# Kernel optimization log

Hardware: AMD Instinct MI355X
Metric: run time of the kernel (lower is better)

## Reference

```python
import jax, jax.numpy as jnp
import numpy as np

D = 1024
H = 16
DFF = 4096
EPS = 1e-5


def layernorm(x, g, b):
    m = jnp.mean(x, axis=-1, keepdims=True)
    v = jnp.var(x, axis=-1, keepdims=True)
    return (x - m) * jax.lax.rsqrt(v + EPS) * g + b


def setup_inputs() -> dict:
    key = jax.random.key(0)
    ks = jax.random.split(key, 6)
    B, T = 2, 2048
    s = 0.02
    return {
        "x": jax.random.normal(ks[0], (B, T, D), dtype=jnp.float32),
        "W_qkv": jax.random.normal(ks[1], (D, 3 * D), dtype=jnp.float32) * s,
        "W_proj": jax.random.normal(ks[2], (D, D), dtype=jnp.float32) * s,
        "W_fc1": jax.random.normal(ks[3], (D, DFF), dtype=jnp.float32) * s,
        "W_fc2": jax.random.normal(ks[4], (DFF, D), dtype=jnp.float32) * s,
        "ln1_g": jnp.ones((D,), jnp.float32),
        "ln1_b": jnp.zeros((D,), jnp.float32),
        "ln2_g": jnp.ones((D,), jnp.float32),
        "ln2_b": jnp.zeros((D,), jnp.float32),
    }


def reference(x, W_qkv, W_proj, W_fc1, W_fc2, ln1_g, ln1_b, ln2_g, ln2_b):
    B, T, C = x.shape
    hd = C // H

    # --- attention sublayer (pre-norm) ---
    h = layernorm(x, ln1_g, ln1_b)
    qkv = h @ W_qkv                                  # [B,T,3C]
    q, k, v = jnp.split(qkv, 3, axis=-1)
    q = q.reshape(B, T, H, hd).transpose(0, 2, 1, 3)  # [B,H,T,hd]
    k = k.reshape(B, T, H, hd).transpose(0, 2, 1, 3)
    v = v.reshape(B, T, H, hd).transpose(0, 2, 1, 3)
    att = jnp.einsum('bhqd,bhkd->bhqk', q, k) * (1.0 / np.sqrt(hd))
    causal = jnp.tril(jnp.ones((T, T), dtype=bool))
    att = jnp.where(causal, att, jnp.float32(-jnp.inf))
    att = jax.nn.softmax(att, axis=-1)
    y = jnp.einsum('bhqk,bhkd->bhqd', att, v)        # [B,H,T,hd]
    y = y.transpose(0, 2, 1, 3).reshape(B, T, C)
    x = x + y @ W_proj

    # --- MLP sublayer (pre-norm) ---
    h = layernorm(x, ln2_g, ln2_b)
    h = jax.nn.gelu(h @ W_fc1, approximate=False)
    x = x + h @ W_fc2
    return x
```

## Files before the change

### kernel.cpp

```cpp
#include <hip/hip_runtime.h>
#include <hip/hip_bf16.h>
#include <math.h>

typedef __bf16 bf16;
typedef __bf16 bf16x4 __attribute__((ext_vector_type(4)));
typedef __bf16 bf16x8 __attribute__((ext_vector_type(8)));
typedef float f32x4 __attribute__((ext_vector_type(4)));
typedef unsigned int u32;

#define MFMA_BF16(a, b, c) __builtin_amdgcn_mfma_f32_16x16x32_bf16(a, b, c, 0, 0, 0)
#define ASYNC16(g, l)                                                                   \
    __builtin_amdgcn_global_load_lds((const __attribute__((address_space(1))) u32*)(g), \
                                     (__attribute__((address_space(3))) u32*)(l), 16, 0, 0)

__global__ __launch_bounds__(256)
void prep_kernel(const float* __restrict__ Wqkv, const float* __restrict__ Wproj,
                 const float* __restrict__ Wfc1, const float* __restrict__ Wfc2,
                 bf16* __restrict__ Wqkvt, bf16* __restrict__ Wprojt,
                 bf16* __restrict__ Wfc1t, bf16* __restrict__ Wfc2t,
                 const float* __restrict__ x, const float* __restrict__ g,
                 const float* __restrict__ bb, bf16* __restrict__ hb) {
    const int blk = blockIdx.x;
    const int tid = threadIdx.x;
    if (blk < 12288) {
        __shared__ float tile[32][33];
        const float* in; bf16* out; int rows, cols, bx, by;
        if (blk < 3072)      { in = Wqkv;  out = Wqkvt;  rows = 1024; cols = 3072; const int r = blk;        bx = r % 96;  by = r / 96; }
        else if (blk < 4096) { in = Wproj; out = Wprojt; rows = 1024; cols = 1024; const int r = blk - 3072; bx = r % 32;  by = r / 32; }
        else if (blk < 8192) { in = Wfc1;  out = Wfc1t;  rows = 1024; cols = 4096; const int r = blk - 4096; bx = r % 128; by = r / 128; }
        else                 { in = Wfc2;  out = Wfc2t;  rows = 4096; cols = 1024; const int r = blk - 8192; bx = r % 32;  by = r / 32; }
        const int tx = tid & 31, ty = tid >> 5;
        const int c0 = bx * 32, r0 = by * 32;
        #pragma unroll
        for (int j = 0; j < 4; j++)
            tile[ty + j * 8][tx] = in[(size_t)(r0 + ty + j * 8) * cols + c0 + tx];
        __syncthreads();
        #pragma unroll
        for (int j = 0; j < 4; j++)
            out[(size_t)(c0 + ty + j * 8) * rows + r0 + tx] = (bf16)tile[tx][ty + j * 8];
    } else {
        const int row = blk - 12288;
        const float4 v = reinterpret_cast<const float4*>(x)[(size_t)row * 256 + tid];
        float s = v.x + v.y + v.z + v.w;
        float sq = v.x * v.x + v.y * v.y + v.z * v.z + v.w * v.w;
        #pragma unroll
        for (int o = 32; o > 0; o >>= 1) { s += __shfl_xor(s, o); sq += __shfl_xor(sq, o); }
        __shared__ float ssum[4], ssq[4];
        const int wave = tid >> 6, lane = tid & 63;
        if (lane == 0) { ssum[wave] = s; ssq[wave] = sq; }
        __syncthreads();
        s = ssum[0] + ssum[1] + ssum[2] + ssum[3];
        sq = ssq[0] + ssq[1] + ssq[2] + ssq[3];
        const float mean = s * (1.0f / 1024.0f);
        const float var = sq * (1.0f / 1024.0f) - mean * mean;
        const float rstd = rsqrtf(var + 1e-5f);
        const float4 gv = reinterpret_cast<const float4*>(g)[tid];
        const float4 bv = reinterpret_cast<const float4*>(bb)[tid];
        bf16x4 o;
        o[0] = (bf16)((v.x - mean) * rstd * gv.x + bv.x);
        o[1] = (bf16)((v.y - mean) * rstd * gv.y + bv.y);
        o[2] = (bf16)((v.z - mean) * rstd * gv.z + bv.z);
        o[3] = (bf16)((v.w - mean) * rstd * gv.w + bv.w);
        reinterpret_cast<bf16x4*>(hb)[(size_t)row * 256 + tid] = o;
    }
}

__global__ __launch_bounds__(256)
void transpose_v(const bf16* __restrict__ qkv, bf16* __restrict__ vt) {
    __shared__ bf16 tile[32][33];
    const int tx = threadIdx.x, ty = threadIdx.y;
    const int t0 = blockIdx.x * 32;
    const int d0 = blockIdx.y * 32;
    const int bh = blockIdx.z;
    const int b = bh >> 4, h = bh & 15;
    const bf16* src = qkv + (size_t)b * 2048 * 3072 + 2048 + h * 64;
    #pragma unroll
    for (int j = 0; j < 4; j++)
        tile[ty + j * 8][tx] = src[(size_t)(t0 + ty + j * 8) * 3072 + d0 + tx];
    __syncthreads();
    #pragma unroll
    for (int j = 0; j < 4; j++)
        vt[((size_t)bh * 64 + d0 + ty + j * 8) * 2048 + t0 + tx] = tile[tx][ty + j * 8];
}

__global__ __launch_bounds__(256)
void ln_kernel(const float* __restrict__ x, const float* __restrict__ g,
               const float* __restrict__ bb, bf16* __restrict__ out) {
    const int row = blockIdx.x, tid = threadIdx.x;
    const float4 v = reinterpret_cast<const float4*>(x)[(size_t)row * 256 + tid];
    float s = v.x + v.y + v.z + v.w;
    float sq = v.x * v.x + v.y * v.y + v.z * v.z + v.w * v.w;
    #pragma unroll
    for (int o = 32; o > 0; o >>= 1) { s += __shfl_xor(s, o); sq += __shfl_xor(sq, o); }
    __shared__ float ssum[4], ssq[4];
    const int wave = tid >> 6, lane = tid & 63;
    if (lane == 0) { ssum[wave] = s; ssq[wave] = sq; }
    __syncthreads();
    s = ssum[0] + ssum[1] + ssum[2] + ssum[3];
    sq = ssq[0] + ssq[1] + ssq[2] + ssq[3];
    const float mean = s * (1.0f / 1024.0f);
    const float var = sq * (1.0f / 1024.0f) - mean * mean;
    const float rstd = rsqrtf(var + 1e-5f);
    const float4 gv = reinterpret_cast<const float4*>(g)[tid];
    const float4 bv = reinterpret_cast<const float4*>(bb)[tid];
    bf16x4 o;
    o[0] = (bf16)((v.x - mean) * rstd * gv.x + bv.x);
    o[1] = (bf16)((v.y - mean) * rstd * gv.y + bv.y);
    o[2] = (bf16)((v.z - mean) * rstd * gv.z + bv.z);
    o[3] = (bf16)((v.w - mean) * rstd * gv.w + bv.w);
    reinterpret_cast<bf16x4*>(out)[(size_t)row * 256 + tid] = o;
}

__device__ __forceinline__ float gelu_fast(float v) {
    const float vv = v * v;
    const float u = v * (1.595769122f + 0.0713548162726f * vv);
    const float t = exp2f(u * -1.4426950408889634f);
    return v / (1.0f + t);
}

template <int EPI>
__global__ __launch_bounds__(512, 1)
void gemm256(const bf16* __restrict__ A, const bf16* __restrict__ Bt,
             bf16* __restrict__ outb, int M, int N, int K) {
    __shared__ bf16 As[2][2][2][128][32];
    __shared__ bf16 Bs[2][2][2][128][32];
    const int tid = threadIdx.x;
    const int wave = tid >> 6, lane = tid & 63;
    const int lm = lane & 15, lq = lane >> 4;
    const int wr = wave >> 2, wc = wave & 3;
    const int bm = blockIdx.y * 256, bn = blockIdx.x * 256;
    const int srow = lane >> 2;
    const int sg = (((lane & 3) ^ ((lane >> 3) & 3)) * 8);
    const int pco = (lq ^ ((lm >> 1) & 3)) * 8;

    f32x4 acc[8][4];
    #pragma unroll
    for (int i = 0; i < 8; i++)
        #pragma unroll
        for (int j = 0; j < 4; j++) acc[i][j] = (f32x4){0.f, 0.f, 0.f, 0.f};

    auto stageA = [&](int db, int kt) {
        #pragma unroll
        for (int L = 0; L < 2; L++) {
            const int g = wave * 2 + L, slab = g >> 3, rg = g & 7;
            #pragma unroll
            for (int h = 0; h < 2; h++)
                ASYNC16(A + (size_t)(bm + h * 128 + rg * 16 + srow) * K + kt + slab * 32 + sg,
                        &As[db][h][slab][rg * 16][0]);
        }
    };
    auto stageB = [&](int db, int kt) {
        #pragma unroll
        for (int L = 0; L < 2; L++) {
            const int g = wave * 2 + L, slab = g >> 3, rg = g & 7;
            #pragma unroll
            for (int h = 0; h < 2; h++)
                ASYNC16(Bt + (size_t)(bn + h * 128 + rg * 16 + srow) * K + kt + slab * 32 + sg,
                        &Bs[db][h][slab][rg * 16][0]);
        }
    };
    auto loadA = [&](int db, int mq, bf16x8 (&dst)[4][2]) {
        #pragma unroll
        for (int i = 0; i < 4; i++)
            #pragma unroll
            for (int kk = 0; kk < 2; kk++)
                dst[i][kk] = *reinterpret_cast<const bf16x8*>(
                    &As[db][wr][kk][(mq * 4 + i) * 16 + lm][pco]);
    };
    auto loadB = [&](int db, int bq, bf16x8 (&dst)[2][2]) {
        #pragma unroll
        for (int j = 0; j < 2; j++)
            #pragma unroll
            for (int kk = 0; kk < 2; kk++)
                dst[j][kk] = *reinterpret_cast<const bf16x8*>(
                    &Bs[db][wc >> 1][kk][(wc & 1) * 64 + (bq * 2 + j) * 16 + lm][pco]);
    };
    auto quad = [&](int mq, int bq, bf16x8 (&a)[4][2], bf16x8 (&b)[2][2]) {
        #pragma unroll
        for (int kk = 0; kk < 2; kk++)
            #pragma unroll
            for (int i = 0; i < 4; i++)
                #pragma unroll
                for (int j = 0; j < 2; j++)
                    acc[mq * 4 + i][bq * 2 + j] =
                        MFMA_BF16(a[i][kk], b[j][kk], acc[mq * 4 + i][bq * 2 + j]);
    };

#define PHASE_SYNC()                                         \
    __builtin_amdgcn_s_barrier();                            \
    asm volatile("s_waitcnt lgkmcnt(0)" ::: "memory");       \
    __builtin_amdgcn_sched_barrier(0)

    const int NT = K >> 6;
    stageB(0, 0);  stageA(0, 0);
    stageB(1, 64); stageA(1, 64);
    asm volatile("s_waitcnt vmcnt(8)" ::: "memory");
    __builtin_amdgcn_s_barrier();
    __builtin_amdgcn_sched_barrier(0);

    bf16x8 af[4][2], b0[2][2], b1[2][2];
    for (int t = 0; t < NT; ++t) {
        const int db = t & 1;
        const int kt2 = (t + 2) * 64;
        loadA(db, 0, af);
        loadB(db, 0, b0);
        PHASE_SYNC();
        __builtin_amdgcn_s_setprio(1);
        quad(0, 0, af, b0);
        __builtin_amdgcn_s_setprio(0);
        __builtin_amdgcn_s_barrier();
        loadB(db, 1, b1);
        PHASE_SYNC();
        __builtin_amdgcn_s_setprio(1);
        quad(0, 1, af, b1);
        __builtin_amdgcn_s_setprio(0);
        __builtin_amdgcn_s_barrier();
        loadA(db, 1, af);
        if (t + 2 < NT) stageB(db, kt2);
        PHASE_SYNC();
        __builtin_amdgcn_s_setprio(1);
        quad(1, 0, af, b0);
        __builtin_amdgcn_s_setprio(0);
        __builtin_amdgcn_s_barrier();
        if (t + 2 < NT) {
            stageA(db, kt2);
            asm volatile("s_waitcnt vmcnt(8)" ::: "memory");
        } else if (t + 1 < NT) {
            asm volatile("s_waitcnt vmcnt(0)" ::: "memory");
        }
        __builtin_amdgcn_s_barrier();
        __builtin_amdgcn_sched_barrier(0);
        __builtin_amdgcn_s_setprio(1);
        quad(1, 1, af, b1);
        __builtin_amdgcn_s_setprio(0);
        __builtin_amdgcn_s_barrier();
    }
#undef PHASE_SYNC

    const int r0 = bm + wr * 128, c0 = bn + wc * 64;
    #pragma unroll
    for (int mi = 0; mi < 8; mi++)
        #pragma unroll
        for (int ni = 0; ni < 4; ni++)
            #pragma unroll
            for (int e = 0; e < 4; e++) {
                const int row = r0 + mi * 16 + lq * 4 + e;
                const int col = c0 + ni * 16 + lm;
                const float v = acc[mi][ni][e];
                const size_t idx = (size_t)row * N + col;
                if (EPI == 0) outb[idx] = (bf16)v;
                else          outb[idx] = (bf16)gelu_fast(v);
            }
}

__global__ __launch_bounds__(512, 2)
void gemm128p(const bf16* __restrict__ A, const bf16* __restrict__ Bt,
              const float* __restrict__ resid, float* __restrict__ outf,
              int M, int N, int K) {
    __shared__ bf16 As[3][128][64];
    __shared__ bf16 Bs[3][128][64];
    const int tid = threadIdx.x;
    const int wave = tid >> 6, lane = tid & 63;
    const int lm = lane & 15, lq = lane >> 4;
    const int wm = (wave >> 2) * 64, wn = (wave & 3) * 32;
    const int nwg = gridDim.x * gridDim.y;
    const int orig = blockIdx.x + gridDim.x * blockIdx.y;
    const int cpx = nwg >> 3;
    const int swz = (orig & 7) * cpx + (orig >> 3);
    const int bx = swz % gridDim.x, by = swz / gridDim.x;
    const int bm = by * 128, bn = bx * 128;
    const int lr8 = lane >> 3;
    const int lg  = ((lane & 7) ^ lr8) * 8;
    const int sa  = lm & 7;
    int co[2];
    co[0] = (lq ^ sa) * 8;
    co[1] = ((lq ^ 4) ^ sa) * 8;
    f32x4 acc[4][2];
    #pragma unroll
    for (int i = 0; i < 4; i++)
        #pragma unroll
        for (int j = 0; j < 2; j++) acc[i][j] = (f32x4){0.f, 0.f, 0.f, 0.f};

    auto stageA = [&](int s, int kt) {
        #pragma unroll
        for (int c = 0; c < 2; c++)
            ASYNC16(A + (size_t)(bm + (wave * 2 + c) * 8 + lr8) * K + kt + lg,
                    &As[s][(wave * 2 + c) * 8][0]);
    };
    auto stageB = [&](int s, int kt) {
        #pragma unroll
        for (int c = 0; c < 2; c++)
            ASYNC16(Bt + (size_t)(bn + (wave * 2 + c) * 8 + lr8) * K + kt + lg,
                    &Bs[s][(wave * 2 + c) * 8][0]);
    };

    const int NT = K >> 6;
    stageA(0, 0);  stageB(0, 0);
    stageA(1, 64); stageB(1, 64);
    asm volatile("s_waitcnt vmcnt(4)" ::: "memory");
    __builtin_amdgcn_s_barrier();
    __builtin_amdgcn_sched_barrier(0);

    int s = 0;
    for (int t = 0; t < NT; ++t) {
        const int s2 = (s + 2 >= 3) ? s - 1 : s + 2;
        const int kt2 = (t + 2) * 64;
        bf16x8 a0[4], b0[2];
        #pragma unroll
        for (int mi = 0; mi < 4; mi++)
            a0[mi] = *reinterpret_cast<const bf16x8*>(&As[s][wm + mi * 16 + lm][co[0]]);
        #pragma unroll
        for (int nj = 0; nj < 2; nj++)
            b0[nj] = *reinterpret_cast<const bf16x8*>(&Bs[s][wn + nj * 16 + lm][co[0]]);
        if (t + 2 < NT) stageA(s2, kt2);
        __builtin_amdgcn_s_barrier();
        asm volatile("s_waitcnt lgkmcnt(0)" ::: "memory");
        __builtin_amdgcn_sched_barrier(0);
        __builtin_amdgcn_s_setprio(1);
        #pragma unroll
        for (int mi = 0; mi < 4; mi++)
            #pragma unroll
            for (int nj = 0; nj < 2; nj++)
                acc[mi][nj] = MFMA_BF16(a0[mi], b0[nj], acc[mi][nj]);
        __builtin_amdgcn_s_setprio(0);
        __builtin_amdgcn_s_barrier();
        #pragma unroll
        for (int mi = 0; mi < 4; mi++)
            a0[mi] = *reinterpret_cast<const bf16x8*>(&As[s][wm + mi * 16 + lm][co[1]]);
        #pragma unroll
        for (int nj = 0; nj < 2; nj++)
            b0[nj] = *reinterpret_cast<const bf16x8*>(&Bs[s][wn + nj * 16 + lm][co[1]]);
        if (t + 2 < NT) {
            stageB(s2, kt2);
            asm volatile("s_waitcnt vmcnt(4)" ::: "memory");
        } else if (t + 1 < NT) {
            asm volatile("s_waitcnt vmcnt(0)" ::: "memory");
        }
        __builtin_amdgcn_s_barrier();
        asm volatile("s_waitcnt lgkmcnt(0)" ::: "memory");
        __builtin_amdgcn_sched_barrier(0);
        __builtin_amdgcn_s_setprio(1);
        #pragma unroll
        for (int mi = 0; mi < 4; mi++)
            #pragma unroll
            for (int nj = 0; nj < 2; nj++)
                acc[mi][nj] = MFMA_BF16(a0[mi], b0[nj], acc[mi][nj]);
        __builtin_amdgcn_s_setprio(0);
        __builtin_amdgcn_s_barrier();
        s = (s == 2) ? 0 : s + 1;
    }

    const int r0 = bm + wm, c0 = bn + wn;
    #pragma unroll
    for (int i = 0; i < 4; i++)
        #pragma unroll
        for (int j = 0; j < 2; j++)
            #pragma unroll
            for (int e = 0; e < 4; e++) {
                const int row = r0 + i * 16 + lq * 4 + e;
                const int col = c0 + j * 16 + lm;
                const size_t idx = (size_t)row * N + col;
                outf[idx] = resid[idx] + acc[i][j][e];
            }
}

__global__ __launch_bounds__(256)
void attn_kernel(const bf16* __restrict__ qkv, const bf16* __restrict__ vt,
                 bf16* __restrict__ y) {
    __shared__ bf16 Ks[64][68];
    __shared__ bf16 Vt[64][68];
    __shared__ bf16 Ps[4][16][68];
    const int tid = threadIdx.x, wave = tid >> 6, lane = tid & 63;
    const int lm = lane & 15, lq = lane >> 4;
    const int h = blockIdx.y, b = blockIdx.z;
    const size_t base = (size_t)b * 2048 * 3072;
    const bf16* Kbase = qkv + base + 1024 + h * 64;
    const bf16* Vbase = vt + ((size_t)(b * 16 + h) * 64) * 2048;
    const int skey = tid >> 3, sch = (tid & 7) * 8;
    const float k1 = 0.18033688011112042f;

    bf16x8 ones;
    #pragma unroll
    for (int j = 0; j < 8; j++) ones[j] = (lm == 0) ? (bf16)1.0f : (bf16)0.0f;

    for (int ph = 0; ph < 2; ph++) {
        const int qt = ph ? (int)blockIdx.x : 31 - (int)blockIdx.x;

        const int qrow = qt * 64 + wave * 16 + lm;
        const bf16* qp = qkv + base + (size_t)qrow * 3072 + h * 64 + lq * 8;
        bf16x8 aq0 = *reinterpret_cast<const bf16x8*>(qp);
        bf16x8 aq1 = *reinterpret_cast<const bf16x8*>(qp + 32);
        #pragma unroll
        for (int j = 0; j < 8; j++) {
            aq0[j] = (bf16)((float)aq0[j] * k1);
            aq1[j] = (bf16)((float)aq1[j] * k1);
        }

        f32x4 Oc[4], Ol;
        #pragma unroll
        for (int nt = 0; nt < 4; nt++) Oc[nt] = (f32x4){0.f, 0.f, 0.f, 0.f};
        Ol = (f32x4){0.f, 0.f, 0.f, 0.f};

        bf16x8 pk0, pk1, pv0, pv1;
        {
            const bf16* kp = Kbase + (size_t)skey * 3072 + sch;
            pk0 = *reinterpret_cast<const bf16x8*>(kp);
            pk1 = *reinterpret_cast<const bf16x8*>(kp + (size_t)32 * 3072);
            const bf16* vp = Vbase + (size_t)skey * 2048 + sch;
            pv0 = *reinterpret_cast<const bf16x8*>(vp);
            pv1 = *reinterpret_cast<const bf16x8*>(vp + (size_t)32 * 2048);
        }

        for (int kt2 = 0; kt2 <= qt; kt2++) {
            __syncthreads();
            *reinterpret_cast<bf16x8*>(&Ks[skey][sch])      = pk0;
            *reinterpret_cast<bf16x8*>(&Ks[skey + 32][sch]) = pk1;
            *reinterpret_cast<bf16x8*>(&Vt[skey][sch])      = pv0;
            *reinterpret_cast<bf16x8*>(&Vt[skey + 32][sch]) = pv1;
            __syncthreads();
            if (kt2 < qt) {
                const bf16* kp = Kbase + (size_t)((kt2 + 1) * 64 + skey) * 3072 + sch;
                pk0 = *reinterpret_cast<const bf16x8*>(kp);
                pk1 = *reinterpret_cast<const bf16x8*>(kp + (size_t)32 * 3072);
                const bf16* vp = Vbase + (size_t)skey * 2048 + (kt2 + 1) * 64 + sch;
                pv0 = *reinterpret_cast<const bf16x8*>(vp);
                pv1 = *reinterpret_cast<const bf16x8*>(vp + (size_t)32 * 2048);
            }

            f32x4 Sc[4];
            #pragma unroll
            for (int nt = 0; nt < 4; nt++) Sc[nt] = (f32x4){0.f, 0.f, 0.f, 0.f};
            #pragma unroll
            for (int nt = 0; nt < 4; nt++) {
                const bf16x8 bk0 = *reinterpret_cast<const bf16x8*>(&Ks[nt * 16 + lm][lq * 8]);
                const bf16x8 bk1 = *reinterpret_cast<const bf16x8*>(&Ks[nt * 16 + lm][32 + lq * 8]);
                Sc[nt] = MFMA_BF16(aq0, bk0, Sc[nt]);
                Sc[nt] = MFMA_BF16(aq1, bk1, Sc[nt]);
            }

            const int qb = wave * 16 + lq * 4;
            #pragma unroll
            for (int e = 0; e < 4; e++) {
                #pragma unroll
                for (int nt = 0; nt < 4; nt++) {
                    float sv = Sc[nt][e];
                    if (kt2 == qt && (nt * 16 + lm) > (qb + e)) sv = -1e30f;
                    Ps[wave][lq * 4 + e][nt * 16 + lm] = (bf16)exp2f(sv);
                }
            }

            const bf16x8 ap0 = *reinterpret_cast<const bf16x8*>(&Ps[wave][lm][lq * 8]);
            const bf16x8 ap1 = *reinterpret_cast<const bf16x8*>(&Ps[wave][lm][32 + lq * 8]);
            Ol = MFMA_BF16(ap0, ones, Ol);
            Ol = MFMA_BF16(ap1, ones, Ol);
            #pragma unroll
            for (int nt = 0; nt < 4; nt++) {
                const bf16x8 bv0 = *reinterpret_cast<const bf16x8*>(&Vt[nt * 16 + lm][lq * 8]);
                const bf16x8 bv1 = *reinterpret_cast<const bf16x8*>(&Vt[nt * 16 + lm][32 + lq * 8]);
                Oc[nt] = MFMA_BF16(ap0, bv0, Oc[nt]);
                Oc[nt] = MFMA_BF16(ap1, bv1, Oc[nt]);
            }
        }

        const int qrow0 = qt * 64 + wave * 16 + lq * 4;
        float inv[4];
        #pragma unroll
        for (int e = 0; e < 4; e++) inv[e] = 1.0f / __shfl(Ol[e], lane & 48);
        #pragma unroll
        for (int nt = 0; nt < 4; nt++)
            #pragma unroll
            for (int e = 0; e < 4; e++) {
                const int row = qrow0 + e;
                y[((size_t)b * 2048 + row) * 1024 + h * 64 + nt * 16 + lm] = (bf16)(Oc[nt][e] * inv[e]);
            }
    }
}

extern "C" void kernel_launch(void* const* d_in, const int* in_sizes, int n_in,
                              void* d_out, int out_size, void* d_ws, size_t ws_size,
                              hipStream_t stream) {
    const float* x     = (const float*)d_in[0];
    const float* Wqkv  = (const float*)d_in[1];
    const float* Wproj = (const float*)d_in[2];
    const float* Wfc1  = (const float*)d_in[3];
    const float* Wfc2  = (const float*)d_in[4];
    const float* ln1g  = (const float*)d_in[5];
    const float* ln1b  = (const float*)d_in[6];
    const float* ln2g  = (const float*)d_in[7];
    const float* ln2b  = (const float*)d_in[8];
    float* out = (float*)d_out;
    char* ws = (char*)d_ws;

    bf16*  Wqkvt  = (bf16*)(ws);
    bf16*  Wprojt = (bf16*)(ws + 6291456);
    bf16*  Wfc1t  = (bf16*)(ws + 8388608);
    bf16*  Wfc2t  = (bf16*)(ws + 16777216);
    bf16*  hb     = (bf16*)(ws + 25165824);
    bf16*  vt     = (bf16*)(ws + 25165824);
    bf16*  qkv    = (bf16*)(ws + 33554432);
    bf16*  yb     = (bf16*)(ws + 58720256);
    float* x1     = (float*)(ws + 67108864);
    bf16*  h3     = (bf16*)(ws + 33554432);

    const dim3 tb(32, 8);
    prep_kernel<<<dim3(16384), dim3(256), 0, stream>>>(Wqkv, Wproj, Wfc1, Wfc2,
                                                       Wqkvt, Wprojt, Wfc1t, Wfc2t,
                                                       x, ln1g, ln1b, hb);
    gemm256<0><<<dim3(12, 16), dim3(512), 0, stream>>>(hb, Wqkvt, qkv, 4096, 3072, 1024);
    transpose_v<<<dim3(64, 2, 32), tb, 0, stream>>>(qkv, vt);
    attn_kernel<<<dim3(16, 16, 2), dim3(256), 0, stream>>>(qkv, vt, yb);
    gemm128p<<<dim3(8, 32), dim3(512), 0, stream>>>(yb, Wprojt, x, x1, 4096, 1024, 1024);
    ln_kernel<<<dim3(4096), dim3(256), 0, stream>>>(x1, ln2g, ln2b, hb);
    gemm256<2><<<dim3(16, 16), dim3(512), 0, stream>>>(hb, Wfc1t, h3, 4096, 4096, 1024);
    gemm128p<<<dim3(8, 32), dim3(512), 0, stream>>>(h3, Wfc2t, x1, out, 4096, 1024, 4096);
}
```

Measured before the change: 325.8 us.

## Split-K the FC2 GEMM with atomic accumulation into residual-initialized output

Replaces the final FC2 GEMM (K=4096, 256 workgroups) with a split-K version that uses two K halves, doubling the grid to 512 workgroups to fill more CUs. The output is first initialized with the residual through a device-to-device memcpy, and each split atomically adds its partial tile. This trades an extra 16MB copy and float atomics (with nondeterministic summation order) for better occupancy and shorter per-block K loops.

```diff
diff --git a/kernel.cpp b/kernel.cpp
--- a/kernel.cpp
+++ b/kernel.cpp
@@ -364,6 +364,106 @@
             }
 }
 
+__global__ __launch_bounds__(512, 2)
+void gemm128sk(const bf16* __restrict__ A, const bf16* __restrict__ Bt,
+               float* __restrict__ outf, int M, int N, int K, int klen) {
+    __shared__ bf16 As[2][128][64];
+    __shared__ bf16 Bs[2][128][64];
+    const int tid = threadIdx.x;
+    const int wave = tid >> 6, lane = tid & 63;
+    const int lm = lane & 15, lq = lane >> 4;
+    const int wm = (wave >> 2) * 64, wn = (wave & 3) * 32;
+    const int nwg = gridDim.x * gridDim.y;
+    const int orig = blockIdx.x + gridDim.x * blockIdx.y;
+    const int cpx = nwg >> 3;
+    const int swz = (orig & 7) * cpx + (orig >> 3);
+    const int bx = swz % gridDim.x, by = swz / gridDim.x;
+    const int bm = by * 128, bn = bx * 128;
+    const int kbase = blockIdx.z * klen;
+    const int lr8 = lane >> 3;
+    const int lg  = ((lane & 7) ^ lr8) * 8;
+    const int sa  = lm & 7;
+    int co[2];
+    co[0] = (lq ^ sa) * 8;
+    co[1] = ((lq ^ 4) ^ sa) * 8;
+    f32x4 acc[4][2];
+    #pragma unroll
+    for (int i = 0; i < 4; i++)
+        #pragma unroll
+        for (int j = 0; j < 2; j++) acc[i][j] = (f32x4){0.f, 0.f, 0.f, 0.f};
+
+    auto stageA = [&](int s, int kt) {
+        #pragma unroll
+        for (int c = 0; c < 2; c++)
+            ASYNC16(A + (size_t)(bm + (wave * 2 + c) * 8 + lr8) * K + kbase + kt + lg,
+                    &As[s][(wave * 2 + c) * 8][0]);
+    };
+    auto stageB = [&](int s, int kt) {
+        #pragma unroll
+        for (int c = 0; c < 2; c++)
+            ASYNC16(Bt + (size_t)(bn + (wave * 2 + c) * 8 + lr8) * K + kbase + kt + lg,
+                    &Bs[s][(wave * 2 + c) * 8][0]);
+    };
+
+    const int NT = klen >> 6;
+    stageA(0, 0);  stageB(0, 0);
+    asm volatile("s_waitcnt vmcnt(0)" ::: "memory");
+    __builtin_amdgcn_s_barrier();
+    __builtin_amdgcn_sched_barrier(0);
+
+    for (int t = 0; t < NT; ++t) {
+        const int s = t & 1;
+        const int kt1 = (t + 1) * 64;
+        if (t + 1 < NT) { stageA(s ^ 1, kt1); stageB(s ^ 1, kt1); }
+        bf16x8 a0[4], b0[2];
+        #pragma unroll
+        for (int mi = 0; mi < 4; mi++)
+            a0[mi] = *reinterpret_cast<const bf16x8*>(&As[s][wm + mi * 16 + lm][co[0]]);
+        #pragma unroll
+        for (int nj = 0; nj < 2; nj++)
+            b0[nj] = *reinterpret_cast<const bf16x8*>(&Bs[s][wn + nj * 16 + lm][co[0]]);
+        asm volatile("s_waitcnt lgkmcnt(0)" ::: "memory");
+        __builtin_amdgcn_sched_barrier(0);
+        __builtin_amdgcn_s_setprio(1);
+        #pragma unroll
+        for (int mi = 0; mi < 4; mi++)
+            #pragma unroll
+            for (int nj = 0; nj < 2; nj++)
+                acc[mi][nj] = MFMA_BF16(a0[mi], b0[nj], acc[mi][nj]);
+        __builtin_amdgcn_s_setprio(0);
+        #pragma unroll
+        for (int mi = 0; mi < 4; mi++)
+            a0[mi] = *reinterpret_cast<const bf16x8*>(&As[s][wm + mi * 16 + lm][co[1]]);
+        #pragma unroll
+        for (int nj = 0; nj < 2; nj++)
+            b0[nj] = *reinterpret_cast<const bf16x8*>(&Bs[s][wn + nj * 16 + lm][co[1]]);
+        asm volatile("s_waitcnt lgkmcnt(0)" ::: "memory");
+        __builtin_amdgcn_sched_barrier(0);
+        __builtin_amdgcn_s_setprio(1);
+        #pragma unroll
+        for (int mi = 0; mi < 4; mi++)
+            #pragma unroll
+            for (int nj = 0; nj < 2; nj++)
+                acc[mi][nj] = MFMA_BF16(a0[mi], b0[nj], acc[mi][nj]);
+        __builtin_amdgcn_s_setprio(0);
+        if (t + 1 < NT) asm volatile("s_waitcnt vmcnt(0)" ::: "memory");
+        __builtin_amdgcn_s_barrier();
+        __builtin_amdgcn_sched_barrier(0);
+    }
+
+    const int r0 = bm + wm, c0 = bn + wn;
+    #pragma unroll
+    for (int i = 0; i < 4; i++)
+        #pragma unroll
+        for (int j = 0; j < 2; j++)
+            #pragma unroll
+            for (int e = 0; e < 4; e++) {
+                const int row = r0 + i * 16 + lq * 4 + e;
+                const int col = c0 + j * 16 + lm;
+                atomicAdd(&outf[(size_t)row * N + col], acc[i][j][e]);
+            }
+}
+
 __global__ __launch_bounds__(256)
 void attn_kernel(const bf16* __restrict__ qkv, const bf16* __restrict__ vt,
                  bf16* __restrict__ y) {
@@ -512,5 +612,6 @@
     gemm128p<<<dim3(8, 32), dim3(512), 0, stream>>>(yb, Wprojt, x, x1, 4096, 1024, 1024);
     ln_kernel<<<dim3(4096), dim3(256), 0, stream>>>(x1, ln2g, ln2b, hb);
     gemm256<2><<<dim3(16, 16), dim3(512), 0, stream>>>(hb, Wfc1t, h3, 4096, 4096, 1024);
-    gemm128p<<<dim3(8, 32), dim3(512), 0, stream>>>(h3, Wfc2t, x1, out, 4096, 1024, 4096);
-}
+    hipMemcpyAsync(out, x1, 16777216, hipMemcpyDeviceToDevice, stream);
+    gemm128sk<<<dim3(8, 32, 2), dim3(512), 0, stream>>>(h3, Wfc2t, out, 4096, 1024, 4096, 2048);
+}
```

Result: slower. 335.7 us (+3.0%).
